# Kernel tuning notes

Hardware: AMD Instinct MI355X
Metric: run time of the kernel (lower is better)

The kernel has to match this reference:

```python
import jax, jax.numpy as jnp
import numpy as np

EMBED_DIM = 4096
NUM_Q_HEADS = 32
NUM_KV_HEADS = 8
HEAD_DIM = EMBED_DIM // NUM_Q_HEADS  # 128
GROUP = NUM_Q_HEADS // NUM_KV_HEADS  # 4
KV_SEQ_LEN = 1024
BATCH = 2
SEQ = 1024
THETA = 10000.0


def _rope(x, positions):
    # x: (B, T, H, D) with interleaved real/imag pairs along D (torch view_as_complex layout)
    half = x.shape[-1] // 2
    inv_freq = 1.0 / (THETA ** (jnp.arange(half, dtype=jnp.float32) / half))
    ang = positions[:, None].astype(jnp.float32) * inv_freq[None, :]  # (T, half)
    cos = jnp.cos(ang)[None, :, None, :].astype(x.dtype)
    sin = jnp.sin(ang)[None, :, None, :].astype(x.dtype)
    xr = x.reshape(*x.shape[:-1], half, 2)
    x0, x1 = xr[..., 0], xr[..., 1]
    o0 = x0 * cos - x1 * sin
    o1 = x0 * sin + x1 * cos
    return jnp.stack([o0, o1], axis=-1).reshape(x.shape)


def setup_inputs() -> dict:
    key = jax.random.key(0)
    ks = jax.random.split(key, 5)
    s_in = 1.0 / np.sqrt(EMBED_DIM)
    return {
        "x": jax.random.normal(ks[0], (BATCH, SEQ, EMBED_DIM), dtype=jnp.float32),
        "Wq": jax.random.normal(ks[1], (EMBED_DIM, EMBED_DIM), dtype=jnp.float32) * s_in,
        "Wk": jax.random.normal(ks[2], (NUM_KV_HEADS * HEAD_DIM, EMBED_DIM), dtype=jnp.float32) * s_in,
        "Wv": jax.random.normal(ks[3], (NUM_KV_HEADS * HEAD_DIM, EMBED_DIM), dtype=jnp.float32) * s_in,
        "Wo": jax.random.normal(ks[4], (EMBED_DIM, EMBED_DIM), dtype=jnp.float32) * s_in,
        "cache_k": jnp.zeros((BATCH, 2 * KV_SEQ_LEN, NUM_KV_HEADS, HEAD_DIM), dtype=jnp.float32),
        "cache_v": jnp.zeros((BATCH, 2 * KV_SEQ_LEN, NUM_KV_HEADS, HEAD_DIM), dtype=jnp.float32),
        "start_pos": 0,
    }


def reference(x, Wq, Wk, Wv, Wo, cache_k, cache_v, start_pos):
    B, T, C = x.shape
    end_pos = start_pos + T
    scale = 1.0 / np.sqrt(HEAD_DIM)

    q = (x @ Wq.T).reshape(B, T, NUM_Q_HEADS, HEAD_DIM)
    k = (x @ Wk.T).reshape(B, T, NUM_KV_HEADS, HEAD_DIM)
    v = (x @ Wv.T).reshape(B, T, NUM_KV_HEADS, HEAD_DIM)

    pos = start_pos + jnp.arange(T)
    q = _rope(q, pos)
    k = _rope(k, pos)

    # KV cache append (writes are detached in the original)
    cache_k = cache_k.at[:, start_pos:end_pos].set(jax.lax.stop_gradient(k))
    cache_v = cache_v.at[:, start_pos:end_pos].set(jax.lax.stop_gradient(v))
    k_full = cache_k[:, :end_pos]  # (B, S, Hkv, D)
    v_full = cache_v[:, :end_pos]

    # GQA without materializing repeated KV heads:
    # q head h attends kv head h // GROUP (matches repeat_interleave layout)
    q5 = q.transpose(0, 2, 1, 3).reshape(B, NUM_KV_HEADS, GROUP, T, HEAD_DIM)
    kh = k_full.transpose(0, 2, 1, 3)  # (B, Hkv, S, D)
    vh = v_full.transpose(0, 2, 1, 3)

    scores = jnp.einsum('bhgtd,bhsd->bhgts', q5, kh) * scale  # (B,Hkv,G,T,S)
    visible = jnp.arange(end_pos)[None, :] <= (start_pos + jnp.arange(T))[:, None]  # (T,S)
    scores = jnp.where(visible[None, None, None], scores, jnp.finfo(scores.dtype).min)
    probs = jax.nn.softmax(scores, axis=-1)
    ctx = jnp.einsum('bhgts,bhsd->bhgtd', probs, vh)

    out = ctx.reshape(B, NUM_Q_HEADS, T, HEAD_DIM).transpose(0, 2, 1, 3).reshape(B, T, C)
    return out @ Wo.T
```

## Files before the change

### kernel.cpp

```cpp
#include <hip/hip_runtime.h>
#include <stdint.h>

typedef unsigned short u16;
typedef __attribute__((ext_vector_type(8))) short short8x;
typedef __attribute__((ext_vector_type(4))) float floatx4;

#define TOKENS 2048
#define EMBED  4096
#define QKVN   6144
#define T_SEQ  1024
#define SMAX   2048
#define NQH    32
#define NKVH   8
#define HD     128

static __device__ __forceinline__ u16 f2b(float f) {
    union { float f; uint32_t u; } v; v.f = f;
    uint32_t r = v.u + 0x7fffu + ((v.u >> 16) & 1u);
    return (u16)(r >> 16);
}
static __device__ __forceinline__ float b2f(u16 h) {
    union { uint32_t u; float f; } v; v.u = ((uint32_t)h) << 16; return v.f;
}

static __device__ __forceinline__ void gload_lds16(const u16* g, u16* l) {
    __builtin_amdgcn_global_load_lds(
        (const __attribute__((address_space(1))) uint32_t*)g,
        (__attribute__((address_space(3))) uint32_t*)l, 16, 0, 0);
}

#define CSEG0 2097152
#define CSEG1 6291456
#define CSEG2 7340032
#define CSEG3 8388608
#define CSEG4 12582912
__global__ void convert_all_kernel(const float* __restrict__ x,  const float* __restrict__ Wq,
                                   const float* __restrict__ Wk, const float* __restrict__ Wv,
                                   const float* __restrict__ Wo,
                                   u16* __restrict__ xb, u16* __restrict__ wqkv,
                                   u16* __restrict__ wob) {
    int i = blockIdx.x * blockDim.x + threadIdx.x;
    if (i >= CSEG4) return;
    const float4* src; uint2* dst; int off;
    if (i < CSEG0)      { src = (const float4*)x;  dst = (uint2*)xb;   off = i; }
    else if (i < CSEG1) { src = (const float4*)Wq; dst = (uint2*)wqkv; off = i - CSEG0; }
    else if (i < CSEG2) { src = (const float4*)Wk; dst = (uint2*)wqkv + 4194304; off = i - CSEG1; }
    else if (i < CSEG3) { src = (const float4*)Wv; dst = (uint2*)wqkv + 5242880; off = i - CSEG2; }
    else                { src = (const float4*)Wo; dst = (uint2*)wob;  off = i - CSEG3; }
    float4 f = src[off];
    union { u16 h[4]; uint2 v; } o;
    o.h[0] = f2b(f.x); o.h[1] = f2b(f.y); o.h[2] = f2b(f.z); o.h[3] = f2b(f.w);
    dst[off] = o.v;
}

#define FENCE asm volatile("" ::: "memory")
#define WAITZ asm volatile("s_waitcnt vmcnt(0)" ::: "memory")
#define NOSTG ((void)0)
#define NOW   ((void)0)

#define HBA(BUF, H) (lds + (BUF) * 28672 + (H) * 8192)
#define HBB(BUF)    (lds + (BUF) * 28672 + 16384)
#define STGA(BUF, H, KT) do { \
    gload_lds16(gA[H][0] + (size_t)(KT) * 64, HBA(BUF, H) + dOffW); \
    gload_lds16(gA[H][1] + (size_t)(KT) * 64, HBA(BUF, H) + 4096 + dOffW); \
} while (0)
#define STGB(BUF, KT) do { \
    _Pragma("unroll") \
    for (int _L = 0; _L < 3; _L++) \
        gload_lds16(gBv[_L] + (size_t)(KT) * 64, HBB(BUF) + _L * 4096 + dOffW); \
} while (0)
#define STGALL(BUF, KT) do { STGA(BUF, 0, KT); STGA(BUF, 1, KT); STGB(BUF, KT); } while (0)
#define PH1(CBUF, STAGES, ENDW) do { \
    const u16* _pa0 = HBA(CBUF, 0); \
    const u16* _pa1 = HBA(CBUF, 1); \
    const u16* _pb  = HBB(CBUF); \
    short8x af0[4][2], af1[4][2], bf[3][2]; \
    _Pragma("unroll") \
    for (int _mi = 0; _mi < 4; _mi++) { \
        af0[_mi][0] = *(const short8x*)(_pa0 + offA[_mi][0]); \
        af0[_mi][1] = *(const short8x*)(_pa0 + offA[_mi][1]); } \
    _Pragma("unroll") \
    for (int _nj = 0; _nj < 3; _nj++) { \
        bf[_nj][0] = *(const short8x*)(_pb + offB[_nj][0]); \
        bf[_nj][1] = *(const short8x*)(_pb + offB[_nj][1]); } \
    STAGES; \
    __builtin_amdgcn_sched_barrier(0); \
    _Pragma("unroll") \
    for (int _mi = 0; _mi < 4; _mi++) { \
        af1[_mi][0] = *(const short8x*)(_pa1 + offA[_mi][0]); \
        af1[_mi][1] = *(const short8x*)(_pa1 + offA[_mi][1]); } \
    __builtin_amdgcn_s_setprio(1); \
    _Pragma("unroll") \
    for (int _kk = 0; _kk < 2; _kk++) \
        _Pragma("unroll") \
        for (int _mi = 0; _mi < 4; _mi++) \
            _Pragma("unroll") \
            for (int _nj = 0; _nj < 3; _nj++) \
                acc[0][_mi][_nj] = __builtin_amdgcn_mfma_f32_16x16x32_bf16( \
                    af0[_mi][_kk], bf[_nj][_kk], acc[0][_mi][_nj], 0, 0, 0); \
    _Pragma("unroll") \
    for (int _kk = 0; _kk < 2; _kk++) \
        _Pragma("unroll") \
        for (int _mi = 0; _mi < 4; _mi++) \
            _Pragma("unroll") \
            for (int _nj = 0; _nj < 3; _nj++) \
                acc[1][_mi][_nj] = __builtin_amdgcn_mfma_f32_16x16x32_bf16( \
                    af1[_mi][_kk], bf[_nj][_kk], acc[1][_mi][_nj], 0, 0, 0); \
    __builtin_amdgcn_s_setprio(0); \
    ENDW; \
    FENCE; __builtin_amdgcn_s_barrier(); FENCE; \
} while (0)

__global__ __launch_bounds__(512, 1) void gemm256_kernel(
    const u16* __restrict__ A, const u16* __restrict__ Bw,
    u16* __restrict__ Cv, int N, int K) {
    extern __shared__ __align__(16) u16 lds[];
    const int tid = threadIdx.x;
    const int lane = tid & 63, w = tid >> 6;
    const int quad = lane >> 4, lc = lane & 15;
    const int wm = w >> 2, wn = w & 3;
    const int Mbase = blockIdx.y * 256, Nbase = blockIdx.x * 192;

    const int r8 = lane >> 3;
    const int sl = (lane & 7) ^ r8;
    const int srow = w * 8 + r8;
    const u16* gA[2][2];
    const u16* gBv[3];
#pragma unroll
    for (int H = 0; H < 2; H++)
#pragma unroll
        for (int L = 0; L < 2; L++)
            gA[H][L] = A + (size_t)(Mbase + H * 128 + L * 64 + srow) * K + sl * 8;
#pragma unroll
    for (int L = 0; L < 3; L++)
        gBv[L] = Bw + (size_t)(Nbase + L * 64 + srow) * K + sl * 8;
    const int dOffW = w * 512;

    int offA[4][2], offB[3][2];
    const int xsw = lc & 7;
#pragma unroll
    for (int mi = 0; mi < 4; mi++)
#pragma unroll
        for (int kk = 0; kk < 2; kk++)
            offA[mi][kk] = (wm * 64 + mi * 16 + lc) * 64 + (((kk * 4 + quad) ^ xsw) * 8);
#pragma unroll
    for (int nj = 0; nj < 3; nj++)
#pragma unroll
        for (int kk = 0; kk < 2; kk++)
            offB[nj][kk] = (wn * 48 + nj * 16 + lc) * 64 + (((kk * 4 + quad) ^ xsw) * 8);

    floatx4 acc[2][4][3] = {};

    STGALL(0, 0);
    WAITZ;
    FENCE; __builtin_amdgcn_s_barrier(); FENCE;

    const int NT = K >> 6;
    for (int t = 0; t < NT - 2; t += 2) {
        PH1(0, STGALL(1, t + 1), WAITZ);
        PH1(1, STGALL(0, t + 2), WAITZ);
    }
    PH1(0, STGALL(1, NT - 1), WAITZ);
    PH1(1, NOSTG, NOW);

#pragma unroll
    for (int AH = 0; AH < 2; AH++)
#pragma unroll
        for (int mi = 0; mi < 4; mi++) {
            const int row0 = Mbase + AH * 128 + wm * 64 + mi * 16 + quad * 4;
#pragma unroll
            for (int nj = 0; nj < 3; nj++) {
                const int col = Nbase + wn * 48 + nj * 16 + lc;
#pragma unroll
                for (int r = 0; r < 4; r++)
                    Cv[(size_t)(row0 + r) * N + col] = f2b(acc[AH][mi][nj][r]);
            }
        }
}
#undef HBA
#undef HBB
#undef STGA
#undef STGB
#undef STGALL
#undef PH1

#define HA2(BUF, H) (lds + (BUF) * 24576 + (H) * 4096)
#define HBB2(BUF)   (lds + (BUF) * 24576 + 8192)
#define STGA2(BUF, H, KT) gload_lds16(gA2[H] + (size_t)(KT) * 64, HA2(BUF, H) + dOffW)
#define STGB2(BUF, KT) do { \
    _Pragma("unroll") \
    for (int _L = 0; _L < 4; _L++) \
        gload_lds16(gB2[_L] + (size_t)(KT) * 64, HBB2(BUF) + _L * 4096 + dOffW); \
} while (0)
#define STGALL2(BUF, KT) do { STGA2(BUF, 0, KT); STGA2(BUF, 1, KT); STGB2(BUF, KT); } while (0)
#define PH2(CBUF, STAGES, ENDW) do { \
    const u16* _pa0 = HA2(CBUF, 0); \
    const u16* _pa1 = HA2(CBUF, 1); \
    const u16* _pb  = HBB2(CBUF); \
    short8x af0[2][2], af1[2][2], bf2[4][2]; \
    _Pragma("unroll") \
    for (int _mi = 0; _mi < 2; _mi++) { \
        af0[_mi][0] = *(const short8x*)(_pa0 + offA2[_mi][0]); \
        af0[_mi][1] = *(const short8x*)(_pa0 + offA2[_mi][1]); } \
    _Pragma("unroll") \
    for (int _nj = 0; _nj < 4; _nj++) { \
        bf2[_nj][0] = *(const short8x*)(_pb + offB2[_nj][0]); \
        bf2[_nj][1] = *(const short8x*)(_pb + offB2[_nj][1]); } \
    STAGES; \
    __builtin_amdgcn_sched_barrier(0); \
    _Pragma("unroll") \
    for (int _mi = 0; _mi < 2; _mi++) { \
        af1[_mi][0] = *(const short8x*)(_pa1 + offA2[_mi][0]); \
        af1[_mi][1] = *(const short8x*)(_pa1 + offA2[_mi][1]); } \
    __builtin_amdgcn_s_setprio(1); \
    _Pragma("unroll") \
    for (int _kk = 0; _kk < 2; _kk++) \
        _Pragma("unroll") \
        for (int _mi = 0; _mi < 2; _mi++) \
            _Pragma("unroll") \
            for (int _nj = 0; _nj < 4; _nj++) \
                acc2[0][_mi][_nj] = __builtin_amdgcn_mfma_f32_16x16x32_bf16( \
                    af0[_mi][_kk], bf2[_nj][_kk], acc2[0][_mi][_nj], 0, 0, 0); \
    _Pragma("unroll") \
    for (int _kk = 0; _kk < 2; _kk++) \
        _Pragma("unroll") \
        for (int _mi = 0; _mi < 2; _mi++) \
            _Pragma("unroll") \
            for (int _nj = 0; _nj < 4; _nj++) \
                acc2[1][_mi][_nj] = __builtin_amdgcn_mfma_f32_16x16x32_bf16( \
                    af1[_mi][_kk], bf2[_nj][_kk], acc2[1][_mi][_nj], 0, 0, 0); \
    __builtin_amdgcn_s_setprio(0); \
    ENDW; \
    FENCE; __builtin_amdgcn_s_barrier(); FENCE; \
} while (0)

__global__ __launch_bounds__(512, 1) void gemmko_kernel(
    const u16* __restrict__ A, const u16* __restrict__ Bw,
    float* __restrict__ C, int N, int K) {
    extern __shared__ __align__(16) u16 lds[];
    const int tid = threadIdx.x;
    const int lane = tid & 63, w = tid >> 6;
    const int quad = lane >> 4, lc = lane & 15;
    const int wm = (w >> 2) & 1, wn = w & 3;
    const int n = blockIdx.x + (blockIdx.y << 4);
    const int by = ((n & 7) << 1) + ((n >> 3) & 1);
    const int bx = n >> 4;
    const int Mbase = by * 128, Nbase = bx * 256;

    const int r8 = lane >> 3;
    const int sl = (lane & 7) ^ r8;
    const int srow = w * 8 + r8;
    const u16* gA2[2];
    const u16* gB2[4];
#pragma unroll
    for (int H = 0; H < 2; H++)
        gA2[H] = A + (size_t)(Mbase + H * 64 + srow) * K + sl * 8;
#pragma unroll
    for (int L = 0; L < 4; L++)
        gB2[L] = Bw + (size_t)(Nbase + L * 64 + srow) * K + sl * 8;
    const int dOffW = w * 512;

    int offA2[2][2], offB2[4][2];
    const int xsw = lc & 7;
#pragma unroll
    for (int mi = 0; mi < 2; mi++)
#pragma unroll
        for (int kk = 0; kk < 2; kk++)
            offA2[mi][kk] = (wm * 32 + mi * 16 + lc) * 64 + (((kk * 4 + quad) ^ xsw) * 8);
#pragma unroll
    for (int nj = 0; nj < 4; nj++)
#pragma unroll
        for (int kk = 0; kk < 2; kk++)
            offB2[nj][kk] = (wn * 64 + nj * 16 + lc) * 64 + (((kk * 4 + quad) ^ xsw) * 8);

    floatx4 acc2[2][2][4] = {};

    STGALL2(0, 0);
    WAITZ;
    FENCE; __builtin_amdgcn_s_barrier(); FENCE;

    const int NT = K >> 6;
    for (int t = 0; t < NT - 2; t += 2) {
        PH2(0, STGALL2(1, t + 1), WAITZ);
        PH2(1, STGALL2(0, t + 2), WAITZ);
    }
    PH2(0, STGALL2(1, NT - 1), WAITZ);
    PH2(1, NOSTG, NOW);

#pragma unroll
    for (int AH = 0; AH < 2; AH++)
#pragma unroll
        for (int mi = 0; mi < 2; mi++) {
            const int row0 = Mbase + AH * 64 + wm * 32 + mi * 16 + quad * 4;
#pragma unroll
            for (int nj = 0; nj < 4; nj++) {
                const int col = Nbase + wn * 64 + nj * 16 + lc;
#pragma unroll
                for (int r = 0; r < 4; r++)
                    C[(size_t)(row0 + r) * N + col] = acc2[AH][mi][nj][r];
            }
        }
}
#undef HA2
#undef HBB2
#undef STGA2
#undef STGB2
#undef STGALL2
#undef PH2
#undef WAITZ
#undef NOSTG
#undef NOW
#undef FENCE

__global__ void cache_prefix_kernel(const float* __restrict__ ck, const float* __restrict__ cv,
                                    const int* __restrict__ sp,
                                    u16* __restrict__ kh, u16* __restrict__ vt8) {
    int spos = sp[0];
    long total = (long)2 * spos * NKVH * HD;
    for (long i = (long)blockIdx.x * blockDim.x + threadIdx.x; i < total; i += (long)gridDim.x * blockDim.x) {
        long d = i % HD, rest = i / HD;
        long g = rest % NKVH; rest /= NKVH;
        long s = rest % spos; long b = rest / spos;
        float kv = ck[((b * SMAX + s) * NKVH + g) * HD + d];
        kh[((b * NKVH + g) * SMAX + s) * HD + d] = f2b(kv);
        float vv = cv[((b * SMAX + s) * NKVH + g) * HD + d];
        vt8[(size_t)(b * NKVH + g) * SMAX * HD + (s >> 3) * 1024 + d * 8 + (s & 7)] = f2b(vv);
    }
}

__global__ void rope_qk_kernel(const u16* __restrict__ qkvb, const int* __restrict__ sp,
                               u16* __restrict__ qh, u16* __restrict__ kh) {
    int spos = sp[0];
    int idx = blockIdx.x * blockDim.x + threadIdx.x;
    int tok = idx / 2560;
    int u = idx - tok * 2560;
    int b = tok >> 10, t = tok & 1023;
    float pos = (float)(spos + t);
    const u16* src = qkvb + (size_t)tok * QKVN;
    const float kScale = 0.08838834764831845f;
    const float kLog = -0.20762050593045857f;
    if (u < 2048) {
        int h = u >> 6, i = u & 63;
        float ang = pos * exp2f((float)i * kLog);
        float cs = cosf(ang), sn = sinf(ang);
        float x0 = b2f(src[h * HD + 2 * i]), x1 = b2f(src[h * HD + 2 * i + 1]);
        size_t dst = (((size_t)(b * NQH + h) * T_SEQ) + t) * HD + 2 * i;
        qh[dst]     = f2b((x0 * cs - x1 * sn) * kScale);
        qh[dst + 1] = f2b((x0 * sn + x1 * cs) * kScale);
    } else {
        int u2 = u - 2048;
        int g = u2 >> 6, i = u2 & 63;
        float ang = pos * exp2f((float)i * kLog);
        float cs = cosf(ang), sn = sinf(ang);
        float x0 = b2f(src[EMBED + g * HD + 2 * i]), x1 = b2f(src[EMBED + g * HD + 2 * i + 1]);
        size_t dst = (((size_t)(b * NKVH + g) * SMAX) + spos + t) * HD + 2 * i;
        kh[dst]     = f2b(x0 * cs - x1 * sn);
        kh[dst + 1] = f2b(x0 * sn + x1 * cs);
    }
}

__global__ __launch_bounds__(256) void vpack_kernel(const u16* __restrict__ qkvb,
                                                    const int* __restrict__ sp,
                                                    u16* __restrict__ vt8) {
    __shared__ u16 lds[16 * 136];
    int spos = sp[0];
    int tile = blockIdx.x;
    int t16 = tile & 63;
    int g = (tile >> 6) & 7;
    int b = tile >> 9;
    int tok0 = t16 * 16;
    int tid = threadIdx.x;
    {
        int srow = tid >> 4, dc8 = (tid & 15) * 8;
        const u16* src = qkvb + (size_t)(b * T_SEQ + tok0 + srow) * QKVN + 5120 + g * HD + dc8;
        *(uint4*)(lds + srow * 136 + dc8) = *(const uint4*)src;
    }
    __syncthreads();
    int d = tid & 127, half = tid >> 7;
    u16* vpg = vt8 + (size_t)(b * NKVH + g) * SMAX * HD;
    int s0 = spos + tok0;
    u16 val[8];
#pragma unroll
    for (int k = 0; k < 8; k++) val[k] = lds[(half * 8 + k) * 136 + d];
    if ((s0 & 7) == 0) {
        union { u16 h[8]; uint4 u; } pk;
#pragma unroll
        for (int k = 0; k < 8; k++) pk.h[k] = val[k];
        *(uint4*)(vpg + (size_t)((s0 >> 3) + half) * 1024 + d * 8) = pk.u;
    } else {
#pragma unroll
        for (int k = 0; k < 8; k++) {
            int s = s0 + half * 8 + k;
            vpg[(size_t)(s >> 3) * 1024 + d * 8 + (s & 7)] = val[k];
        }
    }
}

__global__ __launch_bounds__(256, 2) void attn_kernel(
    const u16* __restrict__ qh, const u16* __restrict__ kh,
    const u16* __restrict__ vt8, const int* __restrict__ sp,
    u16* __restrict__ ctx) {
    extern __shared__ __align__(16) char smem[];
    int spos = sp[0];
    int tid = threadIdx.x, w = tid >> 6, lane = tid & 63;
    int quad = lane >> 4, lc = lane & 15;
    int bid = blockIdx.x;
    int tile = (bid & 7) * 128 + (bid >> 3);
    int j = 63 - (tile & 63);
    int g = (tile >> 6) & 7;
    int b = tile >> 9;
    int qbase = j * 16;

    const u16* kp = kh + (size_t)(b * NKVH + g) * SMAX * HD;
    const u16* vp = vt8 + (size_t)(b * NKVH + g) * SMAX * HD;

    short8x qf[4][4];
#pragma unroll
    for (int m = 0; m < 4; m++) {
        const u16* qp = qh + ((size_t)(b * NQH + g * 4 + m) * T_SEQ + qbase + lc) * HD + quad * 8;
#pragma unroll
        for (int dc = 0; dc < 4; dc++)
            qf[m][dc] = *(const short8x*)(qp + dc * 32);
    }
    short8x ones;
#pragma unroll
    for (int jj = 0; jj < 8; jj++) ones[jj] = (short)0x3F80;

    floatx4 o[4][8] = {};
    floatx4 lacc[4] = {};
    int rowpos = spos + qbase + quad * 4;
    int nch = (spos + qbase + 16 + 63) >> 6;
    u16* pw = (u16*)smem + w * 4608;

    for (int c = w; c < nch; c += 4) {
        int koff = c * 64;
#pragma unroll
        for (int st = 0; st < 4; st++) {
            const u16* kr = kp + (size_t)(koff + st * 16 + lc) * HD + quad * 8;
            floatx4 sc[4] = {};
#pragma unroll
            for (int dc = 0; dc < 4; dc++) {
                short8x kf = *(const short8x*)(kr + dc * 32);
#pragma unroll
                for (int m = 0; m < 4; m++)
                    sc[m] = __builtin_amdgcn_mfma_f32_16x16x32_bf16(qf[m][dc], kf, sc[m], 0, 0, 0);
            }
            int skey = koff + st * 16 + lc;
#pragma unroll
            for (int m = 0; m < 4; m++)
#pragma unroll
                for (int r = 0; r < 4; r++) {
                    float p = (skey <= rowpos + r) ? __expf(sc[m][r]) : 0.0f;
                    pw[m * 1152 + (quad * 4 + r) * 72 + st * 16 + lc] = f2b(p);
                }
        }
        asm volatile("s_waitcnt lgkmcnt(0)" ::: "memory");
#pragma unroll
        for (int hf = 0; hf < 2; hf++) {
            short8x pf[4];
#pragma unroll
            for (int m = 0; m < 4; m++)
                pf[m] = *(const short8x*)(pw + m * 1152 + lc * 72 + hf * 32 + quad * 8);
#pragma unroll
            for (int m = 0; m < 4; m++)
                lacc[m] = __builtin_amdgcn_mfma_f32_16x16x32_bf16(pf[m], ones, lacc[m], 0, 0, 0);
            const u16* vbase = vp + ((size_t)koff << 7) + (size_t)(hf * 4 + quad) * 1024 + lc * 8;
#pragma unroll
            for (int dc8 = 0; dc8 < 8; dc8++) {
                short8x vf = *(const short8x*)(vbase + dc8 * 128);
#pragma unroll
                for (int m = 0; m < 4; m++)
                    o[m][dc8] = __builtin_amdgcn_mfma_f32_16x16x32_bf16(pf[m], vf, o[m][dc8], 0, 0, 0);
            }
        }
    }

    float* obuf = (float*)smem;
    float* lbuf = (float*)(smem + 33792);
    for (int ph = 0; ph < 4; ph++) {
        __syncthreads();
        if (w == ph) {
            if (ph == 0) {
#pragma unroll
                for (int m = 0; m < 4; m++) {
#pragma unroll
                    for (int dc8 = 0; dc8 < 8; dc8++)
#pragma unroll
                        for (int r = 0; r < 4; r++)
                            obuf[(m * 16 + quad * 4 + r) * 132 + dc8 * 16 + lc] = o[m][dc8][r];
#pragma unroll
                    for (int r = 0; r < 4; r++) lbuf[m * 16 + quad * 4 + r] = lacc[m][r];
                }
            } else {
#pragma unroll
                for (int m = 0; m < 4; m++) {
#pragma unroll
                    for (int dc8 = 0; dc8 < 8; dc8++)
#pragma unroll
                        for (int r = 0; r < 4; r++)
                            obuf[(m * 16 + quad * 4 + r) * 132 + dc8 * 16 + lc] += o[m][dc8][r];
#pragma unroll
                    for (int r = 0; r < 4; r++) lbuf[m * 16 + quad * 4 + r] += lacc[m][r];
                }
            }
        }
    }
    __syncthreads();

    int row = tid >> 2;
    int m = row >> 4;
    int cb = (tid & 3) * 32;
    float inv = 1.0f / lbuf[row];
    int token = qbase + (row & 15);
    size_t base = ((size_t)(b * T_SEQ + token) * NQH + g * 4 + m) * HD + cb;
#pragma unroll
    for (int v4 = 0; v4 < 4; v4++) {
        union { u16 h[8]; uint4 u; } pk;
#pragma unroll
        for (int jj = 0; jj < 8; jj++)
            pk.h[jj] = f2b(obuf[row * 132 + cb + v4 * 8 + jj] * inv);
        *(uint4*)(ctx + base + v4 * 8) = pk.u;
    }
}

extern "C" void kernel_launch(void* const* d_in, const int* in_sizes, int n_in,
                              void* d_out, int out_size, void* d_ws, size_t ws_size,
                              hipStream_t stream) {
    const float* x  = (const float*)d_in[0];
    const float* Wq = (const float*)d_in[1];
    const float* Wk = (const float*)d_in[2];
    const float* Wv = (const float*)d_in[3];
    const float* Wo = (const float*)d_in[4];
    const float* ck = (const float*)d_in[5];
    const float* cv = (const float*)d_in[6];
    const int*   sp = (const int*)d_in[7];

    char* p = (char*)d_ws;
    u16* xb   = (u16*)p;
    u16* qh   = xb;
    p += (size_t)TOKENS * EMBED * 2;
    u16* wqkv = (u16*)p; p += (size_t)QKVN * EMBED * 2;
    u16* wob  = (u16*)p; p += (size_t)EMBED * EMBED * 2;
    u16* qkvb = (u16*)p;
    u16* ctx  = qkvb;
    p += (size_t)TOKENS * QKVN * 2;
    u16* kh   = (u16*)p; p += (size_t)2 * NKVH * SMAX * HD * 2;
    u16* vt8  = (u16*)p;

    static int gemm_attr = 0;
    if (!gemm_attr) {
        (void)hipFuncSetAttribute(reinterpret_cast<const void*>(&gemm256_kernel),
                                  hipFuncAttributeMaxDynamicSharedMemorySize, 114688);
        (void)hipFuncSetAttribute(reinterpret_cast<const void*>(&gemmko_kernel),
                                  hipFuncAttributeMaxDynamicSharedMemorySize, 98304);
        (void)hipFuncSetAttribute(reinterpret_cast<const void*>(&attn_kernel),
                                  hipFuncAttributeMaxDynamicSharedMemorySize, 36864);
        gemm_attr = 1;
    }

    convert_all_kernel<<<(CSEG4 + 255) / 256, 256, 0, stream>>>(x, Wq, Wk, Wv, Wo, xb, wqkv, wob);
    gemm256_kernel<<<dim3(QKVN / 192, TOKENS / 256), 512, 114688, stream>>>(xb, wqkv, qkvb, QKVN, EMBED);
    cache_prefix_kernel<<<256, 256, 0, stream>>>(ck, cv, sp, kh, vt8);
    rope_qk_kernel<<<TOKENS * 2560 / 256, 256, 0, stream>>>(qkvb, sp, qh, kh);
    vpack_kernel<<<1024, 256, 0, stream>>>(qkvb, sp, vt8);
    attn_kernel<<<1024, 256, 36864, stream>>>(qh, kh, vt8, sp, ctx);
    gemmko_kernel<<<dim3(EMBED / 256, TOKENS / 128), 512, 98304, stream>>>(ctx, wob, (float*)d_out, EMBED, EMBED);
}
```

Before: 281.4 us.

## Overlap Wo bf16 conversion with attention by adding extra blocks to attention launch

The Wo fp32-to-bf16 conversion moves out of the serial convert kernel and into 512 extra blocks appended to the attention grid, using nontemporal loads and stores. This is meant to hide the memory-bound Wo conversion behind the compute-bound attention tiles instead of running it on the critical path before the QKV GEMM. The risk is that the conversion blocks compete with attention blocks for CU slots and bandwidth, and that the attention tail may grow if they are scheduled late.

```diff
diff --git a/kernel.cpp b/kernel.cpp
--- a/kernel.cpp
+++ b/kernel.cpp
@@ -4,6 +4,8 @@
 typedef unsigned short u16;
 typedef __attribute__((ext_vector_type(8))) short short8x;
 typedef __attribute__((ext_vector_type(4))) float floatx4;
+typedef __attribute__((ext_vector_type(4))) float f32x4;
+typedef __attribute__((ext_vector_type(2))) unsigned int u32x2;
 
 #define TOKENS 2048
 #define EMBED  4096
@@ -33,20 +35,16 @@
 #define CSEG1 6291456
 #define CSEG2 7340032
 #define CSEG3 8388608
-#define CSEG4 12582912
 __global__ void convert_all_kernel(const float* __restrict__ x,  const float* __restrict__ Wq,
                                    const float* __restrict__ Wk, const float* __restrict__ Wv,
-                                   const float* __restrict__ Wo,
-                                   u16* __restrict__ xb, u16* __restrict__ wqkv,
-                                   u16* __restrict__ wob) {
+                                   u16* __restrict__ xb, u16* __restrict__ wqkv) {
     int i = blockIdx.x * blockDim.x + threadIdx.x;
-    if (i >= CSEG4) return;
+    if (i >= CSEG3) return;
     const float4* src; uint2* dst; int off;
     if (i < CSEG0)      { src = (const float4*)x;  dst = (uint2*)xb;   off = i; }
     else if (i < CSEG1) { src = (const float4*)Wq; dst = (uint2*)wqkv; off = i - CSEG0; }
     else if (i < CSEG2) { src = (const float4*)Wk; dst = (uint2*)wqkv + 4194304; off = i - CSEG1; }
-    else if (i < CSEG3) { src = (const float4*)Wv; dst = (uint2*)wqkv + 5242880; off = i - CSEG2; }
-    else                { src = (const float4*)Wo; dst = (uint2*)wob;  off = i - CSEG3; }
+    else                { src = (const float4*)Wv; dst = (uint2*)wqkv + 5242880; off = i - CSEG2; }
     float4 f = src[off];
     union { u16 h[4]; uint2 v; } o;
     o.h[0] = f2b(f.x); o.h[1] = f2b(f.y); o.h[2] = f2b(f.z); o.h[3] = f2b(f.w);
@@ -399,12 +397,26 @@
 __global__ __launch_bounds__(256, 2) void attn_kernel(
     const u16* __restrict__ qh, const u16* __restrict__ kh,
     const u16* __restrict__ vt8, const int* __restrict__ sp,
-    u16* __restrict__ ctx) {
+    u16* __restrict__ ctx,
+    const float* __restrict__ WoF, u16* __restrict__ wob) {
     extern __shared__ __align__(16) char smem[];
+    int tid = threadIdx.x;
+    int bid = blockIdx.x;
+    if (bid >= 1024) {
+        const f32x4* src = (const f32x4*)WoF;
+        u32x2* dst = (u32x2*)wob;
+        for (int i = (bid - 1024) * 256 + tid; i < 4194304; i += 131072) {
+            f32x4 f = __builtin_nontemporal_load(src + i);
+            union { u16 h[4]; u32x2 v; } o;
+            o.h[0] = f2b(f[0]); o.h[1] = f2b(f[1]);
+            o.h[2] = f2b(f[2]); o.h[3] = f2b(f[3]);
+            __builtin_nontemporal_store(o.v, dst + i);
+        }
+        return;
+    }
     int spos = sp[0];
-    int tid = threadIdx.x, w = tid >> 6, lane = tid & 63;
+    int w = tid >> 6, lane = tid & 63;
     int quad = lane >> 4, lc = lane & 15;
-    int bid = blockIdx.x;
     int tile = (bid & 7) * 128 + (bid >> 3);
     int j = 63 - (tile & 63);
     int g = (tile >> 6) & 7;
@@ -558,11 +570,11 @@
         gemm_attr = 1;
     }
 
-    convert_all_kernel<<<(CSEG4 + 255) / 256, 256, 0, stream>>>(x, Wq, Wk, Wv, Wo, xb, wqkv, wob);
+    convert_all_kernel<<<(CSEG3 + 255) / 256, 256, 0, stream>>>(x, Wq, Wk, Wv, xb, wqkv);
     gemm256_kernel<<<dim3(QKVN / 192, TOKENS / 256), 512, 114688, stream>>>(xb, wqkv, qkvb, QKVN, EMBED);
     cache_prefix_kernel<<<256, 256, 0, stream>>>(ck, cv, sp, kh, vt8);
     rope_qk_kernel<<<TOKENS * 2560 / 256, 256, 0, stream>>>(qkvb, sp, qh, kh);
     vpack_kernel<<<1024, 256, 0, stream>>>(qkvb, sp, vt8);
-    attn_kernel<<<1024, 256, 36864, stream>>>(qh, kh, vt8, sp, ctx);
+    attn_kernel<<<1536, 256, 36864, stream>>>(qh, kh, vt8, sp, ctx, Wo, wob);
     gemmko_kernel<<<dim3(EMBED / 256, TOKENS / 128), 512, 98304, stream>>>(ctx, wob, (float*)d_out, EMBED, EMBED);
 }
```

New measurement: 301.7 us. 7.2% more time.
